# Performance work log

Measured on AMD Instinct MI355X. Metric: run time of the kernel, lower is better.

## Reference

```python
import jax, jax.numpy as jnp
import numpy as np

B, T, N, M, D = 4, 64, 16, 8, 512

def setup_inputs() -> dict:
    key = jax.random.key(0)
    ks = jax.random.split(key, 7)
    s = 1.0 / np.sqrt(D)
    return {
        "x": jax.random.normal(ks[0], (B, T, N, M, D), dtype=jnp.float32),
        "Wq": jax.random.normal(ks[1], (D, D), dtype=jnp.float32) * s,
        "bq": jax.random.normal(ks[2], (D,), dtype=jnp.float32) * s,
        "Wk": jax.random.normal(ks[3], (D, D), dtype=jnp.float32) * s,
        "bk": jax.random.normal(ks[4], (D,), dtype=jnp.float32) * s,
        "Wv": jax.random.normal(ks[5], (D, D), dtype=jnp.float32) * s,
        "bv": jax.random.normal(ks[6], (D,), dtype=jnp.float32) * s,
    }

def reference(x, Wq, bq, Wk, bk, Wv, bv):
    # Linear projections (torch Linear: y = x @ W^T + b)
    Q = jnp.einsum('btnmd,ed->btnme', x, Wq) + bq
    K = jnp.einsum('btnmd,ed->btnme', x, Wk) + bk
    V = jnp.einsum('btnmd,ed->btnme', x, Wv) + bv
    scale = 1.0 / jnp.sqrt(jnp.asarray(Q.shape[-1], Q.dtype))
    # contract over batch b AND feature d -> shared attention over modality axis m
    attn_score = jnp.einsum('btnmd,btnkd->tnmk', Q, K) * scale  # [t,n,m,m]
    attn_weight = jax.nn.softmax(attn_score, axis=-1)
    return jnp.einsum('tnmk,btnkd->btnmd', attn_weight, V)
```

## Files before the change

kernel.cpp:

```cpp
#include <hip/hip_runtime.h>

#define Bb 4
#define Tt 64
#define Nn 16
#define Mm 8
#define Dd 512
#define RR 32
#define QSTR 520

typedef __attribute__((ext_vector_type(8))) short bf16x8;
typedef __attribute__((ext_vector_type(16))) float f32x16;

__device__ __forceinline__ unsigned short f2bf(float f) {
    union { float f; unsigned int u; } v; v.f = f;
    unsigned int r = (v.u + 0x7fffu + ((v.u >> 16) & 1u)) >> 16;
    return (unsigned short)r;
}
__device__ __forceinline__ float bf2f(unsigned short h) {
    union { unsigned int u; float f; } v; v.u = ((unsigned int)h) << 16;
    return v.f;
}

__global__ __launch_bounds__(256) void convert_w_kernel(
    const float* __restrict__ Wq, const float* __restrict__ Wk,
    const float* __restrict__ Wv, unsigned short* __restrict__ Wb)
{
    int idx = blockIdx.x * 256 + threadIdx.x;
    int o = idx << 2;
    int j  = o & 7;
    int n  = (o >> 3) & 31;
    int hi = (o >> 8) & 1;
    int ekk = o >> 9;
    int kk = ekk & 31;
    int e  = ekk >> 5;
    int row = e * 32 + n;
    int d = kk * 16 + hi * 8 + j;
    const float* src = (row < 512) ? Wq : ((row < 1024) ? Wk : Wv);
    int r = row & 511;
    float4 v = *(const float4*)(src + r * Dd + d);
    ushort4 o4;
    o4.x = f2bf(v.x); o4.y = f2bf(v.y); o4.z = f2bf(v.z); o4.w = f2bf(v.w);
    *(ushort4*)(Wb + o) = o4;
}

__global__ __launch_bounds__(1024, 4) void fused_attn_kernel(
    const float* __restrict__ x, const unsigned short* __restrict__ Wb,
    const float* __restrict__ bq, const float* __restrict__ bk,
    const float* __restrict__ bv, float* __restrict__ out)
{
    __shared__ unsigned short lds_x[2][RR * QSTR];
    __shared__ float lds_s[2][64];

    const int tid = threadIdx.x;
    const int lane = tid & 63;
    const int wave = tid >> 6;
    const int arow = lane & 31;
    const int ahalf = lane >> 5;

    const int gi0 = blockIdx.x << 1;
    const int t = gi0 >> 4;
    const int n0 = gi0 & 15;

    const unsigned short* wq = Wb + ((long)wave << 14) + (lane << 3);
    const unsigned short* wk = wq + (16L << 14);
    bf16x8 pq[2], pk[2];
    pq[0] = *(const bf16x8*)(wq);
    pk[0] = *(const bf16x8*)(wk);
    pq[1] = *(const bf16x8*)(wq + 512);
    pk[1] = *(const bf16x8*)(wk + 512);

    if (tid < 128) lds_s[tid >> 6][tid & 63] = 0.f;

    #pragma unroll
    for (int i = 0; i < 8; ++i) {
        int fi = i * 1024 + tid;
        int g = fi >> 12;
        int rem = fi & 4095;
        int row = rem >> 7;
        int d = (rem & 127) << 2;
        int b = row >> 3, m = row & 7;
        float4 v = *(const float4*)(x + ((((long)(b * Tt + t)) * Nn + (n0 + g)) * Mm + m) * Dd + d);
        ushort4 o;
        o.x = f2bf(v.x); o.y = f2bf(v.y); o.z = f2bf(v.z); o.w = f2bf(v.w);
        *(ushort4*)(&lds_x[g][row * QSTR + d]) = o;
    }
    __syncthreads();

    const unsigned short* abase0 = &lds_x[0][arow * QSTR + (ahalf << 3)];
    const unsigned short* abase1 = &lds_x[1][arow * QSTR + (ahalf << 3)];

    f32x16 aQ0, aQ1, aK0, aK1;
    #pragma unroll
    for (int r = 0; r < 16; ++r) { aQ0[r] = 0.f; aQ1[r] = 0.f; aK0[r] = 0.f; aK1[r] = 0.f; }

    #pragma unroll
    for (int kk = 0; kk < 32; ++kk) {
        int cur = kk & 1;
        bf16x8 wqf = pq[cur];
        bf16x8 wkf = pk[cur];
        if (kk < 30) {
            pq[cur] = *(const bf16x8*)(wq + (kk + 2) * 512);
            pk[cur] = *(const bf16x8*)(wk + (kk + 2) * 512);
        }
        bf16x8 a0 = *(const bf16x8*)(abase0 + kk * 16);
        bf16x8 a1 = *(const bf16x8*)(abase1 + kk * 16);
        aQ0 = __builtin_amdgcn_mfma_f32_32x32x16_bf16(a0, wqf, aQ0, 0, 0, 0);
        aK0 = __builtin_amdgcn_mfma_f32_32x32x16_bf16(a0, wkf, aK0, 0, 0, 0);
        aQ1 = __builtin_amdgcn_mfma_f32_32x32x16_bf16(a1, wqf, aQ1, 0, 0, 0);
        aK1 = __builtin_amdgcn_mfma_f32_32x32x16_bf16(a1, wkf, aK1, 0, 0, 0);
    }
    {
        int f = (wave << 5) + arow;
        float bqv = bq[f], bkv = bk[f];
        #pragma unroll
        for (int r = 0; r < 16; ++r) {
            aQ0[r] += bqv; aQ1[r] += bqv;
            aK0[r] += bkv; aK1[r] += bkv;
        }
    }

    auto scores = [&](const f32x16& aQ, const f32x16& aK, int g) {
        float ksw[16];
        #pragma unroll
        for (int r = 0; r < 16; ++r) ksw[r] = __shfl_xor(aK[r], 32);
        #pragma unroll
        for (int j = 0; j < 4; ++j) {
            float v0 = 0.f, v1 = 0.f, v2 = 0.f, v3 = 0.f;
            float v4 = 0.f, v5 = 0.f, v6 = 0.f, v7 = 0.f;
            #pragma unroll
            for (int b = 0; b < 4; ++b) {
                float qv = aQ[b * 4 + j];
                v0 += qv * aK[b * 4 + 0];  v1 += qv * aK[b * 4 + 1];
                v2 += qv * aK[b * 4 + 2];  v3 += qv * aK[b * 4 + 3];
                v4 += qv * ksw[b * 4 + 0]; v5 += qv * ksw[b * 4 + 1];
                v6 += qv * ksw[b * 4 + 2]; v7 += qv * ksw[b * 4 + 3];
            }
            const bool s0 = (lane & 1) != 0;
            const bool s1 = (lane & 2) != 0;
            const bool s2 = (lane & 4) != 0;
            float n0v = (s0 ? v4 : v0) + __shfl_xor(s0 ? v0 : v4, 1);
            float n1v = (s0 ? v5 : v1) + __shfl_xor(s0 ? v1 : v5, 1);
            float n2v = (s0 ? v6 : v2) + __shfl_xor(s0 ? v2 : v6, 1);
            float n3v = (s0 ? v7 : v3) + __shfl_xor(s0 ? v3 : v7, 1);
            float m0v = (s1 ? n2v : n0v) + __shfl_xor(s1 ? n0v : n2v, 2);
            float m1v = (s1 ? n3v : n1v) + __shfl_xor(s1 ? n1v : n3v, 2);
            float u   = (s2 ? m1v : m0v) + __shfl_xor(s2 ? m0v : m1v, 4);
            u += __shfl_xor(u, 8);
            u += __shfl_xor(u, 16);
            int l5 = lane & 31;
            if (l5 < 8) {
                int slot = (l5 & 1) * 4 + (l5 & 2) + ((l5 >> 2) & 1);
                int m = 4 * ahalf + j;
                int k = (slot < 4) ? (4 * ahalf + slot) : (4 * (1 - ahalf) + (slot - 4));
                atomicAdd(&lds_s[g][m * 8 + k], u);
            }
        }
    };
    scores(aQ0, aK0, 0);
    scores(aQ1, aK1, 1);

    const unsigned short* wv = Wb + ((32L + wave) << 14) + (lane << 3);
    bf16x8 pv[4];
    #pragma unroll
    for (int i = 0; i < 4; ++i) pv[i] = *(const bf16x8*)(wv + i * 512);

    __syncthreads();

    if (tid < 128) {
        int g = tid >> 6;
        int p = tid & 63;
        float s = lds_s[g][p] * 0.04419417382415922f;
        float mx = s;
        mx = fmaxf(mx, __shfl_xor(mx, 1));
        mx = fmaxf(mx, __shfl_xor(mx, 2));
        mx = fmaxf(mx, __shfl_xor(mx, 4));
        float e = __expf(s - mx);
        float sum = e;
        sum += __shfl_xor(sum, 1);
        sum += __shfl_xor(sum, 2);
        sum += __shfl_xor(sum, 4);
        lds_s[g][p] = e / sum;
    }
    __syncthreads();

    {
        int d4 = tid & 127;
        int b = (tid >> 7) & 3;
        int g = tid >> 9;
        unsigned short* xr = &lds_x[g][(b << 3) * QSTR + (d4 << 2)];
        float4 xv[8];
        #pragma unroll
        for (int k = 0; k < 8; ++k) {
            ushort4 u = *(const ushort4*)(xr + k * QSTR);
            xv[k].x = bf2f(u.x); xv[k].y = bf2f(u.y);
            xv[k].z = bf2f(u.z); xv[k].w = bf2f(u.w);
        }
        ushort4 yr[8];
        #pragma unroll
        for (int m = 0; m < 8; ++m) {
            float4 o = {0.f, 0.f, 0.f, 0.f};
            #pragma unroll
            for (int k = 0; k < 8; ++k) {
                float w = lds_s[g][(m << 3) + k];
                o.x += w * xv[k].x; o.y += w * xv[k].y;
                o.z += w * xv[k].z; o.w += w * xv[k].w;
            }
            ushort4 oy;
            oy.x = f2bf(o.x); oy.y = f2bf(o.y); oy.z = f2bf(o.z); oy.w = f2bf(o.w);
            yr[m] = oy;
        }
        #pragma unroll
        for (int m = 0; m < 8; ++m) *(ushort4*)(xr + m * QSTR) = yr[m];
    }
    __syncthreads();

    {
        f32x16 aV0, aV1;
        #pragma unroll
        for (int r = 0; r < 16; ++r) { aV0[r] = 0.f; aV1[r] = 0.f; }
        #pragma unroll
        for (int kk = 0; kk < 32; ++kk) {
            int cur = kk & 3;
            bf16x8 wvf = pv[cur];
            if (kk < 28) pv[cur] = *(const bf16x8*)(wv + (kk + 4) * 512);
            bf16x8 a0 = *(const bf16x8*)(abase0 + kk * 16);
            bf16x8 a1 = *(const bf16x8*)(abase1 + kk * 16);
            aV0 = __builtin_amdgcn_mfma_f32_32x32x16_bf16(a0, wvf, aV0, 0, 0, 0);
            aV1 = __builtin_amdgcn_mfma_f32_32x32x16_bf16(a1, wvf, aV1, 0, 0, 0);
        }
        int f = (wave << 5) + arow;
        float bvv = bv[f];
        float* o0 = out + f;
        #pragma unroll
        for (int r = 0; r < 16; ++r) {
            int mrow = (r & 3) + 8 * (r >> 2) + 4 * ahalf;
            int b = mrow >> 3, m = mrow & 7;
            long base = ((((long)(b * Tt + t)) * Nn + n0) * Mm + m) * Dd;
            o0[base] = aV0[r] + bvv;
            o0[base + (long)Mm * Dd] = aV1[r] + bvv;
        }
    }
}

extern "C" void kernel_launch(void* const* d_in, const int* in_sizes, int n_in,
                              void* d_out, int out_size, void* d_ws, size_t ws_size,
                              hipStream_t stream) {
    const float* x  = (const float*)d_in[0];
    const float* Wq = (const float*)d_in[1];
    const float* bq = (const float*)d_in[2];
    const float* Wk = (const float*)d_in[3];
    const float* bk = (const float*)d_in[4];
    const float* Wv = (const float*)d_in[5];
    const float* bv = (const float*)d_in[6];
    float* out = (float*)d_out;
    unsigned short* Wb = (unsigned short*)d_ws;

    convert_w_kernel<<<768, 256, 0, stream>>>(Wq, Wk, Wv, Wb);
    fused_attn_kernel<<<Tt * Nn / 2, 1024, 0, stream>>>(x, Wb, bq, bk, bv, out);
}
```

Measured before the change: 194.6 us.

## Fold Wq^T·Wk into one precomputed matrix to halve QK projection MFMAs

Replaces the separate Q and K projections with a single projection through a precomputed bf16 product of Wq^T and Wk, plus a Wk^T·bq bias row. The bias row is fed through a constant-one column appended to x in LDS. Terms that are constant across k drop out, which is exact because softmax is shift-invariant, and this roughly halves the MFMA work before the scores. A new pack kernel does a 512³ fp32 matmul on every call, and rounding the weight product to bf16 can change numerics. Weight-fetch k-order is rotated per block to spread cache and memory traffic, and the LDS row stride is padded.

```diff
diff --git a/kernel.cpp b/kernel.cpp
--- a/kernel.cpp
+++ b/kernel.cpp
@@ -6,7 +6,8 @@
 #define Mm 8
 #define Dd 512
 #define RR 32
-#define QSTR 520
+#define QSTR 536
+#define VOFF 270336
 
 typedef __attribute__((ext_vector_type(8))) short bf16x8;
 typedef __attribute__((ext_vector_type(16))) float f32x16;
@@ -21,8 +22,7 @@
     return v.f;
 }
 
-__global__ __launch_bounds__(256) void convert_w_kernel(
-    const float* __restrict__ Wq, const float* __restrict__ Wk,
+__global__ __launch_bounds__(256) void pack_wv_kernel(
     const float* __restrict__ Wv, unsigned short* __restrict__ Wb)
 {
     int idx = blockIdx.x * 256 + threadIdx.x;
@@ -35,17 +35,72 @@
     int e  = ekk >> 5;
     int row = e * 32 + n;
     int d = kk * 16 + hi * 8 + j;
-    const float* src = (row < 512) ? Wq : ((row < 1024) ? Wk : Wv);
-    int r = row & 511;
-    float4 v = *(const float4*)(src + r * Dd + d);
+    float4 v = *(const float4*)(Wv + row * Dd + d);
     ushort4 o4;
     o4.x = f2bf(v.x); o4.y = f2bf(v.y); o4.z = f2bf(v.z); o4.w = f2bf(v.w);
-    *(ushort4*)(Wb + o) = o4;
+    *(ushort4*)(Wb + VOFF + o) = o4;
+}
+
+__global__ __launch_bounds__(256) void pack_bqk_kernel(
+    const float* __restrict__ Wq, const float* __restrict__ Wk,
+    const float* __restrict__ bq, unsigned short* __restrict__ Wb)
+{
+    __shared__ unsigned short lq[512 * 32];
+    __shared__ unsigned short lk[512 * 32];
+    const int tid = threadIdx.x;
+    const int eT = blockIdx.x & 15;
+    const int dT = blockIdx.x >> 4;
+
+    #pragma unroll
+    for (int i = 0; i < 16; ++i) {
+        int fi = i * 256 + tid;
+        int n = fi >> 3;
+        int c4 = (fi & 7) << 2;
+        float4 vq = *(const float4*)(Wq + n * Dd + dT * 32 + c4);
+        float4 vk = *(const float4*)(Wk + n * Dd + eT * 32 + c4);
+        ushort4 a, b;
+        a.x = f2bf(vq.x); a.y = f2bf(vq.y); a.z = f2bf(vq.z); a.w = f2bf(vq.w);
+        b.x = f2bf(vk.x); b.y = f2bf(vk.y); b.z = f2bf(vk.z); b.w = f2bf(vk.w);
+        *(ushort4*)(&lq[n * 32 + c4]) = a;
+        *(ushort4*)(&lk[n * 32 + c4]) = b;
+    }
+    __syncthreads();
+
+    {
+        int dp = tid & 31;
+        int e0 = (tid >> 5) << 2;
+        float acc0 = 0.f, acc1 = 0.f, acc2 = 0.f, acc3 = 0.f;
+        for (int n = 0; n < 512; ++n) {
+            float a = bf2f(lq[n * 32 + dp]);
+            acc0 += a * bf2f(lk[n * 32 + e0 + 0]);
+            acc1 += a * bf2f(lk[n * 32 + e0 + 1]);
+            acc2 += a * bf2f(lk[n * 32 + e0 + 2]);
+            acc3 += a * bf2f(lk[n * 32 + e0 + 3]);
+        }
+        int kk = dT * 2 + (dp >> 4);
+        int k16 = dp & 15;
+        int h = k16 >> 3, j = k16 & 7;
+        long base = ((long)(eT * 33 + kk) << 9) + ((h * 32) << 3) + j;
+        Wb[base + ((e0 + 0) << 3)] = f2bf(acc0);
+        Wb[base + ((e0 + 1) << 3)] = f2bf(acc1);
+        Wb[base + ((e0 + 2) << 3)] = f2bf(acc2);
+        Wb[base + ((e0 + 3) << 3)] = f2bf(acc3);
+    }
+
+    if (dT == 0) {
+        long b32 = (long)(eT * 33 + 32) << 9;
+        if (tid < 256) { Wb[b32 + tid] = 0; Wb[b32 + 256 + tid] = 0; }
+        __syncthreads();
+        if (tid < 32) {
+            float c = 0.f;
+            for (int n = 0; n < 512; ++n) c += bf2f(lk[n * 32 + tid]) * bq[n];
+            Wb[b32 + (tid << 3)] = f2bf(c);
+        }
+    }
 }
 
 __global__ __launch_bounds__(1024, 4) void fused_attn_kernel(
     const float* __restrict__ x, const unsigned short* __restrict__ Wb,
-    const float* __restrict__ bq, const float* __restrict__ bk,
     const float* __restrict__ bv, float* __restrict__ out)
 {
     __shared__ unsigned short lds_x[2][RR * QSTR];
@@ -56,18 +111,21 @@
     const int wave = tid >> 6;
     const int arow = lane & 31;
     const int ahalf = lane >> 5;
+    const int l5 = lane & 31;
 
     const int gi0 = blockIdx.x << 1;
     const int t = gi0 >> 4;
     const int n0 = gi0 & 15;
-
-    const unsigned short* wq = Wb + ((long)wave << 14) + (lane << 3);
-    const unsigned short* wk = wq + (16L << 14);
-    bf16x8 pq[2], pk[2];
-    pq[0] = *(const bf16x8*)(wq);
-    pk[0] = *(const bf16x8*)(wk);
-    pq[1] = *(const bf16x8*)(wq + 512);
-    pk[1] = *(const bf16x8*)(wk + 512);
+    const int rot = (blockIdx.x * 7) & 31;
+
+    const unsigned short* wb = Wb + (long)wave * (33 * 512) + (lane << 3);
+    #define KOF(s) ((s) + rot >= 32 ? (s) + rot - 32 : (s) + rot)
+
+    bf16x8 pf[4];
+    pf[0] = *(const bf16x8*)(wb + KOF(0) * 512);
+    pf[1] = *(const bf16x8*)(wb + KOF(1) * 512);
+    pf[2] = *(const bf16x8*)(wb + KOF(2) * 512);
+    pf[3] = *(const bf16x8*)(wb + KOF(3) * 512);
 
     if (tid < 128) lds_s[tid >> 6][tid & 63] = 0.f;
 
@@ -84,85 +142,101 @@
         o.x = f2bf(v.x); o.y = f2bf(v.y); o.z = f2bf(v.z); o.w = f2bf(v.w);
         *(ushort4*)(&lds_x[g][row * QSTR + d]) = o;
     }
+    if (tid < 64) {
+        int g = tid >> 5, row = tid & 31;
+        unsigned short* p = &lds_x[g][row * QSTR + 512];
+        ushort4 one = {0x3F80, 0, 0, 0}, zz = {0, 0, 0, 0};
+        *(ushort4*)(p) = one; *(ushort4*)(p + 4) = zz;
+        *(ushort4*)(p + 8) = zz; *(ushort4*)(p + 12) = zz;
+    }
     __syncthreads();
 
     const unsigned short* abase0 = &lds_x[0][arow * QSTR + (ahalf << 3)];
     const unsigned short* abase1 = &lds_x[1][arow * QSTR + (ahalf << 3)];
 
-    f32x16 aQ0, aQ1, aK0, aK1;
-    #pragma unroll
-    for (int r = 0; r < 16; ++r) { aQ0[r] = 0.f; aQ1[r] = 0.f; aK0[r] = 0.f; aK1[r] = 0.f; }
-
-    #pragma unroll
-    for (int kk = 0; kk < 32; ++kk) {
-        int cur = kk & 1;
-        bf16x8 wqf = pq[cur];
-        bf16x8 wkf = pk[cur];
-        if (kk < 30) {
-            pq[cur] = *(const bf16x8*)(wq + (kk + 2) * 512);
-            pk[cur] = *(const bf16x8*)(wk + (kk + 2) * 512);
+    f32x16 aY0, aY1;
+    #pragma unroll
+    for (int r = 0; r < 16; ++r) { aY0[r] = 0.f; aY1[r] = 0.f; }
+
+    #pragma unroll
+    for (int s = 0; s < 33; ++s) {
+        int kk = (s < 32) ? KOF(s) : 32;
+        bf16x8 bf = pf[s & 3];
+        if (s + 4 <= 32) {
+            int kn = (s + 4 < 32) ? KOF(s + 4) : 32;
+            pf[s & 3] = *(const bf16x8*)(wb + kn * 512);
         }
         bf16x8 a0 = *(const bf16x8*)(abase0 + kk * 16);
         bf16x8 a1 = *(const bf16x8*)(abase1 + kk * 16);
-        aQ0 = __builtin_amdgcn_mfma_f32_32x32x16_bf16(a0, wqf, aQ0, 0, 0, 0);
-        aK0 = __builtin_amdgcn_mfma_f32_32x32x16_bf16(a0, wkf, aK0, 0, 0, 0);
-        aQ1 = __builtin_amdgcn_mfma_f32_32x32x16_bf16(a1, wqf, aQ1, 0, 0, 0);
-        aK1 = __builtin_amdgcn_mfma_f32_32x32x16_bf16(a1, wkf, aK1, 0, 0, 0);
-    }
-    {
-        int f = (wave << 5) + arow;
-        float bqv = bq[f], bkv = bk[f];
-        #pragma unroll
-        for (int r = 0; r < 16; ++r) {
-            aQ0[r] += bqv; aQ1[r] += bqv;
-            aK0[r] += bkv; aK1[r] += bkv;
-        }
-    }
-
-    auto scores = [&](const f32x16& aQ, const f32x16& aK, int g) {
-        float ksw[16];
-        #pragma unroll
-        for (int r = 0; r < 16; ++r) ksw[r] = __shfl_xor(aK[r], 32);
-        #pragma unroll
-        for (int j = 0; j < 4; ++j) {
-            float v0 = 0.f, v1 = 0.f, v2 = 0.f, v3 = 0.f;
-            float v4 = 0.f, v5 = 0.f, v6 = 0.f, v7 = 0.f;
+        aY0 = __builtin_amdgcn_mfma_f32_32x32x16_bf16(a0, bf, aY0, 0, 0, 0);
+        aY1 = __builtin_amdgcn_mfma_f32_32x32x16_bf16(a1, bf, aY1, 0, 0, 0);
+    }
+
+    const int ecol = (wave << 5) + l5;
+    #pragma unroll
+    for (int g = 0; g < 2; ++g) {
+        const f32x16& aY = g ? aY1 : aY0;
+        float p[32];
+        #pragma unroll
+        for (int i = 0; i < 32; ++i) p[i] = 0.f;
+        #pragma unroll
+        for (int b = 0; b < 4; ++b) {
+            float xc[8];
             #pragma unroll
-            for (int b = 0; b < 4; ++b) {
-                float qv = aQ[b * 4 + j];
-                v0 += qv * aK[b * 4 + 0];  v1 += qv * aK[b * 4 + 1];
-                v2 += qv * aK[b * 4 + 2];  v3 += qv * aK[b * 4 + 3];
-                v4 += qv * ksw[b * 4 + 0]; v5 += qv * ksw[b * 4 + 1];
-                v6 += qv * ksw[b * 4 + 2]; v7 += qv * ksw[b * 4 + 3];
+            for (int k = 0; k < 8; ++k)
+                xc[k] = bf2f(lds_x[g][(b * 8 + k) * QSTR + ecol]);
+            #pragma unroll
+            for (int mm = 0; mm < 4; ++mm) {
+                float yv = aY[b * 4 + mm];
+                #pragma unroll
+                for (int k = 0; k < 8; ++k) p[mm * 8 + k] += yv * xc[k];
             }
-            const bool s0 = (lane & 1) != 0;
-            const bool s1 = (lane & 2) != 0;
-            const bool s2 = (lane & 4) != 0;
-            float n0v = (s0 ? v4 : v0) + __shfl_xor(s0 ? v0 : v4, 1);
-            float n1v = (s0 ? v5 : v1) + __shfl_xor(s0 ? v1 : v5, 1);
-            float n2v = (s0 ? v6 : v2) + __shfl_xor(s0 ? v2 : v6, 1);
-            float n3v = (s0 ? v7 : v3) + __shfl_xor(s0 ? v3 : v7, 1);
-            float m0v = (s1 ? n2v : n0v) + __shfl_xor(s1 ? n0v : n2v, 2);
-            float m1v = (s1 ? n3v : n1v) + __shfl_xor(s1 ? n1v : n3v, 2);
-            float u   = (s2 ? m1v : m0v) + __shfl_xor(s2 ? m0v : m1v, 4);
-            u += __shfl_xor(u, 8);
-            u += __shfl_xor(u, 16);
-            int l5 = lane & 31;
-            if (l5 < 8) {
-                int slot = (l5 & 1) * 4 + (l5 & 2) + ((l5 >> 2) & 1);
-                int m = 4 * ahalf + j;
-                int k = (slot < 4) ? (4 * ahalf + slot) : (4 * (1 - ahalf) + (slot - 4));
-                atomicAdd(&lds_s[g][m * 8 + k], u);
-            }
-        }
-    };
-    scores(aQ0, aK0, 0);
-    scores(aQ1, aK1, 1);
-
-    const unsigned short* wv = Wb + ((32L + wave) << 14) + (lane << 3);
+        }
+        const bool b0 = (lane & 1) != 0;
+        const bool b1 = (lane & 2) != 0;
+        const bool b2 = (lane & 4) != 0;
+        const bool b3 = (lane & 8) != 0;
+        const bool b4 = (lane & 16) != 0;
+        float q16[16];
+        #pragma unroll
+        for (int i = 0; i < 16; ++i) {
+            float keep = b0 ? p[2 * i + 1] : p[2 * i];
+            float send = b0 ? p[2 * i] : p[2 * i + 1];
+            q16[i] = keep + __shfl_xor(send, 1);
+        }
+        float q8[8];
+        #pragma unroll
+        for (int i = 0; i < 8; ++i) {
+            float keep = b1 ? q16[2 * i + 1] : q16[2 * i];
+            float send = b1 ? q16[2 * i] : q16[2 * i + 1];
+            q8[i] = keep + __shfl_xor(send, 2);
+        }
+        float q4[4];
+        #pragma unroll
+        for (int i = 0; i < 4; ++i) {
+            float keep = b2 ? q8[2 * i + 1] : q8[2 * i];
+            float send = b2 ? q8[2 * i] : q8[2 * i + 1];
+            q4[i] = keep + __shfl_xor(send, 4);
+        }
+        float q2[2];
+        #pragma unroll
+        for (int i = 0; i < 2; ++i) {
+            float keep = b3 ? q4[2 * i + 1] : q4[2 * i];
+            float send = b3 ? q4[2 * i] : q4[2 * i + 1];
+            q2[i] = keep + __shfl_xor(send, 8);
+        }
+        float sval = (b4 ? q2[1] : q2[0]) + __shfl_xor(b4 ? q2[0] : q2[1], 16);
+        int k = l5 & 7, mm = l5 >> 3;
+        int m = mm + 4 * ahalf;
+        atomicAdd(&lds_s[g][m * 8 + k], sval);
+    }
+
+    const unsigned short* vb = Wb + VOFF + ((long)wave << 14) + (lane << 3);
     bf16x8 pv[4];
-    #pragma unroll
-    for (int i = 0; i < 4; ++i) pv[i] = *(const bf16x8*)(wv + i * 512);
+    pv[0] = *(const bf16x8*)(vb + ((0 + rot) & 31) * 512);
+    pv[1] = *(const bf16x8*)(vb + ((1 + rot) & 31) * 512);
+    pv[2] = *(const bf16x8*)(vb + ((2 + rot) & 31) * 512);
+    pv[3] = *(const bf16x8*)(vb + ((3 + rot) & 31) * 512);
 
     __syncthreads();
 
@@ -219,10 +293,10 @@
         #pragma unroll
         for (int r = 0; r < 16; ++r) { aV0[r] = 0.f; aV1[r] = 0.f; }
         #pragma unroll
-        for (int kk = 0; kk < 32; ++kk) {
-            int cur = kk & 3;
-            bf16x8 wvf = pv[cur];
-            if (kk < 28) pv[cur] = *(const bf16x8*)(wv + (kk + 4) * 512);
+        for (int s = 0; s < 32; ++s) {
+            int kk = (s + rot) & 31;
+            bf16x8 wvf = pv[s & 3];
+            if (s + 4 < 32) pv[s & 3] = *(const bf16x8*)(vb + (((s + 4 + rot) & 31)) * 512);
             bf16x8 a0 = *(const bf16x8*)(abase0 + kk * 16);
             bf16x8 a1 = *(const bf16x8*)(abase1 + kk * 16);
             aV0 = __builtin_amdgcn_mfma_f32_32x32x16_bf16(a0, wvf, aV0, 0, 0, 0);
@@ -240,6 +314,7 @@
             o0[base + (long)Mm * Dd] = aV1[r] + bvv;
         }
     }
+    #undef KOF
 }
 
 extern "C" void kernel_launch(void* const* d_in, const int* in_sizes, int n_in,
@@ -249,12 +324,12 @@
     const float* Wq = (const float*)d_in[1];
     const float* bq = (const float*)d_in[2];
     const float* Wk = (const float*)d_in[3];
-    const float* bk = (const float*)d_in[4];
+    const float* bv = (const float*)d_in[6];
     const float* Wv = (const float*)d_in[5];
-    const float* bv = (const float*)d_in[6];
     float* out = (float*)d_out;
     unsigned short* Wb = (unsigned short*)d_ws;
 
-    convert_w_kernel<<<768, 256, 0, stream>>>(Wq, Wk, Wv, Wb);
-    fused_attn_kernel<<<Tt * Nn / 2, 1024, 0, stream>>>(x, Wb, bq, bk, bv, out);
-}
+    pack_wv_kernel<<<256, 256, 0, stream>>>(Wv, Wb);
+    pack_bqk_kernel<<<256, 256, 0, stream>>>(Wq, Wk, bq, Wb);
+    fused_attn_kernel<<<Tt * Nn / 2, 1024, 0, stream>>>(x, Wb, bv, out);
+}
```

Result: slower. 201.7 us (+3.7%).
